# Optimization experiments

Hardware: AMD Instinct MI355X
Metric: run time of the kernel (lower is better)

Reference implementation:

```python
import jax, jax.numpy as jnp
import numpy as np

N_NODES = 50000
N_EDGES = 1600000
N_GRAPHS = 16
K_SLOTS = 8
LATENT = 4
HID = 32


def _linear(key, fan_in, fan_out):
    lim = 1.0 / np.sqrt(fan_in)
    kw, kb = jax.random.split(key)
    w = jax.random.uniform(kw, (fan_in, fan_out), minval=-lim, maxval=lim, dtype=jnp.float32)
    b = jax.random.uniform(kb, (fan_out,), minval=-lim, maxval=lim, dtype=jnp.float32)
    return w, b


def setup_inputs() -> dict:
    key = jax.random.key(0)
    ks = jax.random.split(key, 12)
    x = jax.random.normal(ks[0], (N_NODES, 4), dtype=jnp.float32)
    pos = jax.random.normal(ks[1], (N_NODES, 3), dtype=jnp.float32)
    # edge_index without self-loops (src != dst) so dist > 0 everywhere
    src = jax.random.randint(ks[2], (N_EDGES,), 0, N_NODES)
    off = jax.random.randint(ks[3], (N_EDGES,), 1, N_NODES)
    dst = (src + off) % N_NODES
    edge_index = jnp.stack([src, dst], axis=0).astype(jnp.int64)
    batch = jnp.sort(jax.random.randint(ks[4], (N_NODES,), 0, N_GRAPHS)).astype(jnp.int64)
    enc_w1, enc_b1 = _linear(ks[5], 4 * 2 + 1, HID)
    enc_w2, enc_b2 = _linear(ks[6], HID, HID)
    pool_w, pool_b = _linear(ks[7], HID, K_SLOTS)
    toz_w, toz_b = _linear(ks[8], HID, LATENT)
    dec_w1, dec_b1 = _linear(ks[9], LATENT, HID)
    dec_w2, dec_b2 = _linear(ks[10], HID, 4)
    return {
        "x": x, "pos": pos, "edge_index": edge_index, "batch": batch,
        "enc_w1": enc_w1, "enc_b1": enc_b1, "enc_w2": enc_w2, "enc_b2": enc_b2,
        "pool_w": pool_w, "pool_b": pool_b, "toz_w": toz_w, "toz_b": toz_b,
        "dec_w1": dec_w1, "dec_b1": dec_b1, "dec_w2": dec_w2, "dec_b2": dec_b2,
    }


def reference(x, pos, edge_index, batch,
              enc_w1, enc_b1, enc_w2, enc_b2,
              pool_w, pool_b, toz_w, toz_b,
              dec_w1, dec_b1, dec_w2, dec_b2):
    src = edge_index[0]  # x_j (source)
    dst = edge_index[1]  # x_i (target, aggregation index in PyG default flow)
    # EquiLayer: relative distance + message MLP + mean aggregation
    rel_pos = pos[src] - pos[dst]                         # [E, 3]
    dist = jnp.linalg.norm(rel_pos, axis=-1, keepdims=True)  # [E, 1]
    msg_in = jnp.concatenate([x[dst], x[src], dist], axis=-1)  # [E, 9]
    msg = jax.nn.silu(msg_in @ enc_w1 + enc_b1) @ enc_w2 + enc_b2  # [E, 32]
    summed = jax.ops.segment_sum(msg, dst, num_segments=N_NODES)   # [N, 32]
    cnt = jax.ops.segment_sum(jnp.ones((msg.shape[0], 1), msg.dtype), dst,
                              num_segments=N_NODES)
    h = summed / jnp.maximum(cnt, 1.0)                    # scatter-mean
    # soft pooling over k slots per graph
    s = jax.nn.softmax(h @ pool_w + pool_b, axis=-1)      # [N, k]
    pooled_h = jax.ops.segment_sum(s[:, :, None] * h[:, None, :], batch,
                                   num_segments=N_GRAPHS)  # [B, k, 32]
    z = pooled_h @ toz_w + toz_b                           # [B, k, latent]
    # decode: torch.matmul(s [N,k], z [B,k,d]) -> [B, N, d]
    q = jnp.einsum('nk,bkd->bnd', s, z)
    recon = jax.nn.silu(q @ dec_w1 + dec_b1) @ dec_w2 + dec_b2  # [B, N, 4]
    return recon
```

## Files before the change

### kernel.cpp

```cpp
#include <hip/hip_runtime.h>
#include <hip/hip_bf16.h>

#define N_NODES 50000
#define N_EDGES 1600000
#define N_GRAPHS 16
#define K_SLOTS 8
#define LATENT 4
#define HID 32
#define NBUCKET 196
#define BCAP 10240
#define BIN_EPB 4096

typedef __hip_bfloat16 bf16;
typedef __attribute__((ext_vector_type(8))) short short8;
typedef __attribute__((ext_vector_type(4))) float f32x4;

__device__ __forceinline__ float ldf(const void* p, long i, int isbf) {
    return isbf ? __bfloat162float(((const bf16*)p)[i]) : ((const float*)p)[i];
}
__device__ __forceinline__ int ldi(const int* p, long i, int is64) {
    return is64 ? p[2 * i] : p[i];
}
__device__ __forceinline__ short f2bs(float f) {
    bf16 h = __float2bfloat16(f);
    return *reinterpret_cast<short*>(&h);
}
__device__ __forceinline__ float bs2f(unsigned s) {
    union { unsigned u; float f; } cv;
    cv.u = (s & 0xFFFFu) << 16;
    return cv.f;
}
__device__ __forceinline__ float fast_silu(float v) {
    return v * __builtin_amdgcn_rcpf(1.f + __expf(-v));
}

#define WS_HSUM 0
#define WS_POOL (N_NODES * HID)
#define WS_GFILL (WS_POOL + N_GRAPHS * K_SLOTS * HID)
#define WS_ZERO_CNT (WS_GFILL + 256)
#define WS_S    (WS_GFILL + 256)
#define WS_FRAGS (WS_S + N_NODES * K_SLOTS)
#define WS_DEG  (WS_FRAGS + 1024)
#define WS_BINNED (WS_DEG + N_NODES)
#define WS_EDAT (WS_BINNED + NBUCKET * BCAP)
#define WS_FLAGS (WS_EDAT + N_EDGES)

__global__ void prep_kernel(const void* x, const int* ei,
                            const void* w1, const void* w2,
                            int* flags, short* frags)
{
    int t = threadIdx.x;
    unsigned short h = ((const unsigned short*)x)[2 * t];
    unsigned e = (h >> 7) & 0xFF;
    bool sane = ((h & 0x7FFF) == 0 || (e >= 100 && e <= 141));
    unsigned long long bs = __ballot(sane);
    int f0 = (__popcll(bs) >= 32) ? 1 : 0;
    bool z = (ei[2 * t + 1] == 0);
    unsigned long long bz = __ballot(z);
    int f1 = (__popcll(bz) >= 60) ? 1 : 0;
    if (t == 0) { flags[0] = f0; flags[1] = f1; }

    int fbf = f0;
    int nl = t & 15, quad = (t >> 4) & 3;
#pragma unroll
    for (int j = 0; j < 8; j++) {
        int k = quad * 8 + j;
        frags[(0 * 64 + t) * 8 + j] = (k < 9) ? f2bs(ldf(w1, k * 32 + nl, fbf)) : (short)0;
        frags[(1 * 64 + t) * 8 + j] = (k < 9) ? f2bs(ldf(w1, k * 32 + 16 + nl, fbf)) : (short)0;
        frags[(2 * 64 + t) * 8 + j] = f2bs(ldf(w2, k * 32 + nl, fbf));
        frags[(3 * 64 + t) * 8 + j] = f2bs(ldf(w2, k * 32 + 16 + nl, fbf));
    }
}

__global__ __launch_bounds__(256) void bin_kernel(
    const int* __restrict__ ei, int* __restrict__ gfill,
    unsigned* __restrict__ binned, const int* __restrict__ flags)
{
    const int i64 = flags[1];
    __shared__ int cnt[NBUCKET];
    __shared__ int cur[NBUCKET];
    int t = threadIdx.x;
    for (int i = t; i < NBUCKET; i += 256) cnt[i] = 0;
    __syncthreads();

    long e0 = (long)blockIdx.x * BIN_EPB;
    unsigned pk[16];
    if (!i64) {
#pragma unroll
        for (int kk = 0; kk < 4; kk++) {
            long e = e0 + kk * 1024 + t * 4;
            if (e < N_EDGES) {
                int4 sv = *(const int4*)(ei + e);
                int4 dv = *(const int4*)(ei + N_EDGES + e);
                pk[kk * 4 + 0] = (unsigned)sv.x | ((unsigned)dv.x << 16);
                pk[kk * 4 + 1] = (unsigned)sv.y | ((unsigned)dv.y << 16);
                pk[kk * 4 + 2] = (unsigned)sv.z | ((unsigned)dv.z << 16);
                pk[kk * 4 + 3] = (unsigned)sv.w | ((unsigned)dv.w << 16);
                atomicAdd(&cnt[dv.x >> 8], 1);
                atomicAdd(&cnt[dv.y >> 8], 1);
                atomicAdd(&cnt[dv.z >> 8], 1);
                atomicAdd(&cnt[dv.w >> 8], 1);
            } else {
                pk[kk * 4 + 0] = pk[kk * 4 + 1] = pk[kk * 4 + 2] = pk[kk * 4 + 3] = 0xFFFFFFFFu;
            }
        }
    } else {
#pragma unroll
        for (int kk = 0; kk < 8; kk++) {
            long e = e0 + kk * 512 + t * 2;
            if (e < N_EDGES) {
                int4 sv = *(const int4*)(ei + 2 * e);
                int4 dv = *(const int4*)(ei + 2 * (N_EDGES + e));
                pk[kk * 2 + 0] = (unsigned)sv.x | ((unsigned)dv.x << 16);
                pk[kk * 2 + 1] = (unsigned)sv.z | ((unsigned)dv.z << 16);
                atomicAdd(&cnt[dv.x >> 8], 1);
                atomicAdd(&cnt[dv.z >> 8], 1);
            } else {
                pk[kk * 2 + 0] = pk[kk * 2 + 1] = 0xFFFFFFFFu;
            }
        }
    }
    __syncthreads();
    for (int i = t; i < NBUCKET; i += 256)
        cur[i] = atomicAdd(&gfill[i], cnt[i]);
    __syncthreads();
    int nk = i64 ? 16 : 16;
#pragma unroll
    for (int k = 0; k < 16; k++) {
        if (k < nk && pk[k] != 0xFFFFFFFFu) {
            int b = pk[k] >> 24;
            int pos = atomicAdd(&cur[b], 1);
            binned[(long)b * BCAP + pos] = pk[k];
        }
    }
}

__global__ __launch_bounds__(1024) void csr_kernel(
    const int* __restrict__ gfill, const unsigned* __restrict__ binned,
    unsigned* __restrict__ edat, int* __restrict__ deg)
{
    __shared__ int gsm[256];
    __shared__ int lcnt[256], lcur[256], sm[256];
    int b = blockIdx.x, t = threadIdx.x;
    if (t < 256) gsm[t] = (t < NBUCKET) ? gfill[t] : 0;
    if (t < 256) lcnt[t] = 0;
    __syncthreads();
    for (int s = 1; s < 256; s <<= 1) {
        int v = 0;
        if (t < 256) v = gsm[t] + ((t >= s) ? gsm[t - s] : 0);
        __syncthreads();
        if (t < 256) gsm[t] = v;
        __syncthreads();
    }
    int cnt = gfill[b];
    int base = gsm[b] - cnt;
    const unsigned* bp = binned + (long)b * BCAP;
    for (int i = t; i < cnt; i += 1024)
        atomicAdd(&lcnt[(bp[i] >> 16) & 255], 1);
    __syncthreads();
    if (t < 256) sm[t] = lcnt[t];
    __syncthreads();
    for (int s = 1; s < 256; s <<= 1) {
        int v = 0;
        if (t < 256) v = sm[t] + ((t >= s) ? sm[t - s] : 0);
        __syncthreads();
        if (t < 256) sm[t] = v;
        __syncthreads();
    }
    if (t < 256) {
        lcur[t] = sm[t] - lcnt[t];
        int n = b * 256 + t;
        if (n < N_NODES) deg[n] = lcnt[t];
    }
    __syncthreads();
    for (int i = t; i < cnt; i += 1024) {
        unsigned pk = bp[i];
        int pos = base + atomicAdd(&lcur[(pk >> 16) & 255], 1);
        edat[pos] = pk;
    }
}

__global__ __launch_bounds__(256) void msg_agg_kernel(
    const void* __restrict__ x, const void* __restrict__ pos,
    const unsigned* __restrict__ edat, const short* __restrict__ frags,
    const void* __restrict__ b1, const void* __restrict__ b2,
    float* __restrict__ hsum, const int* __restrict__ flags)
{
    const int fbf = flags[0];
    __shared__ short buf[256 * 34];
    __shared__ int sdL[256];
    __shared__ int runstart[256];
    __shared__ int wcnt[4];

    int t = threadIdx.x;
    int lane = t & 63, wv = t >> 6;
    int nl = lane & 15, quad = lane >> 4;

    const short8 w1f0 = *(const short8*)&frags[(0 * 64 + lane) * 8];
    const short8 w1f1 = *(const short8*)&frags[(1 * 64 + lane) * 8];
    const short8 w2f0 = *(const short8*)&frags[(2 * 64 + lane) * 8];
    const short8 w2f1 = *(const short8*)&frags[(3 * 64 + lane) * 8];
    float b1c0 = ldf(b1, nl, fbf), b1c1 = ldf(b1, 16 + nl, fbf);
    float b2c0 = ldf(b2, nl, fbf), b2c1 = ldf(b2, 16 + nl, fbf);

    long i = (long)blockIdx.x * 256 + t;
    unsigned ed = edat[i];
    int src = (int)(ed & 0xFFFFu);
    int dst = (int)(ed >> 16);
    sdL[t] = dst;

    float in[9];
    if (fbf) {
        const unsigned* xb = (const unsigned*)x;
        unsigned d0 = xb[dst * 2], d1 = xb[dst * 2 + 1];
        unsigned s0 = xb[src * 2], s1 = xb[src * 2 + 1];
        in[0] = bs2f(d0); in[1] = bs2f(d0 >> 16);
        in[2] = bs2f(d1); in[3] = bs2f(d1 >> 16);
        in[4] = bs2f(s0); in[5] = bs2f(s0 >> 16);
        in[6] = bs2f(s1); in[7] = bs2f(s1 >> 16);
        const unsigned short* pp = (const unsigned short*)pos;
        float dx = bs2f(pp[3 * src + 0]) - bs2f(pp[3 * dst + 0]);
        float dy = bs2f(pp[3 * src + 1]) - bs2f(pp[3 * dst + 1]);
        float dz = bs2f(pp[3 * src + 2]) - bs2f(pp[3 * dst + 2]);
        in[8] = sqrtf(dx * dx + dy * dy + dz * dz);
    } else {
        float4 xd = ((const float4*)x)[dst];
        float4 xs = ((const float4*)x)[src];
        in[0] = xd.x; in[1] = xd.y; in[2] = xd.z; in[3] = xd.w;
        in[4] = xs.x; in[5] = xs.y; in[6] = xs.z; in[7] = xs.w;
        const float* pf = (const float*)pos;
        float dx = pf[3 * src + 0] - pf[3 * dst + 0];
        float dy = pf[3 * src + 1] - pf[3 * dst + 1];
        float dz = pf[3 * src + 2] - pf[3 * dst + 2];
        in[8] = sqrtf(dx * dx + dy * dy + dz * dz);
    }

    {
        unsigned* rowp = (unsigned*)&buf[t * 34];
        short v9 = f2bs(in[8]);
        rowp[0] = (unsigned)(unsigned short)f2bs(in[0]) | ((unsigned)(unsigned short)f2bs(in[1]) << 16);
        rowp[1] = (unsigned)(unsigned short)f2bs(in[2]) | ((unsigned)(unsigned short)f2bs(in[3]) << 16);
        rowp[2] = (unsigned)(unsigned short)f2bs(in[4]) | ((unsigned)(unsigned short)f2bs(in[5]) << 16);
        rowp[3] = (unsigned)(unsigned short)f2bs(in[6]) | ((unsigned)(unsigned short)f2bs(in[7]) << 16);
        rowp[4] = (unsigned)(unsigned short)v9;
#pragma unroll
        for (int p = 5; p < 16; p++) rowp[p] = 0;
    }
    __syncthreads();

    int rb = wv * 64;
    short8 af[4];
#pragma unroll
    for (int mt = 0; mt < 4; mt++) {
        int row = rb + mt * 16 + nl;
        af[mt] = *(short8*)&buf[row * 34 + quad * 8];
    }
    __syncthreads();

    f32x4 zero = {0.f, 0.f, 0.f, 0.f};
#pragma unroll
    for (int mt = 0; mt < 4; mt++) {
        f32x4 c0 = __builtin_amdgcn_mfma_f32_16x16x32_bf16(af[mt], w1f0, zero, 0, 0, 0);
        f32x4 c1 = __builtin_amdgcn_mfma_f32_16x16x32_bf16(af[mt], w1f1, zero, 0, 0, 0);
#pragma unroll
        for (int r = 0; r < 4; r++) {
            int row = rb + mt * 16 + quad * 4 + r;
            buf[row * 34 + nl] = f2bs(fast_silu(c0[r] + b1c0));
            buf[row * 34 + 16 + nl] = f2bs(fast_silu(c1[r] + b1c1));
        }
    }
    __syncthreads();

    short8 a2f[4];
#pragma unroll
    for (int mt = 0; mt < 4; mt++) {
        int row = rb + mt * 16 + nl;
        a2f[mt] = *(short8*)&buf[row * 34 + quad * 8];
    }
    __syncthreads();

    short* msgT = buf;
#pragma unroll
    for (int mt = 0; mt < 4; mt++) {
        f32x4 d0 = __builtin_amdgcn_mfma_f32_16x16x32_bf16(a2f[mt], w2f0, zero, 0, 0, 0);
        f32x4 d1 = __builtin_amdgcn_mfma_f32_16x16x32_bf16(a2f[mt], w2f1, zero, 0, 0, 0);
#pragma unroll
        for (int r = 0; r < 4; r++) {
            int orow = rb + mt * 16 + quad * 4 + r;
            msgT[nl * 258 + orow] = f2bs(d0[r] + b2c0);
            msgT[(nl + 16) * 258 + orow] = f2bs(d1[r] + b2c1);
        }
    }
    __syncthreads();

    bool head = (t == 0) || (sdL[t] != sdL[t - 1]);
    unsigned long long bal = __ballot(head);
    if (lane == 0) wcnt[wv] = __popcll(bal);
    __syncthreads();
    int nruns = wcnt[0] + wcnt[1] + wcnt[2] + wcnt[3];
    if (head) {
        int base = 0;
        for (int q = 0; q < wv; q++) base += wcnt[q];
        int myrun = base + __popcll(bal & (((unsigned long long)1 << lane) - 1ull));
        runstart[myrun] = t;
    }
    __syncthreads();

    int g = t >> 5, c = t & 31;
    const short* col = &msgT[c * 258];
    const unsigned* colu = (const unsigned*)col;
    for (int r = g; r < nruns; r += 8) {
        int s0 = runstart[r];
        int s1 = (r + 1 < nruns) ? runstart[r + 1] : 256;
        float acc = 0.f;
        int j = s0;
        if (j & 1) { acc += bs2f((unsigned)(unsigned short)col[j]); j++; }
        for (; j + 1 < s1; j += 2) {
            unsigned d = colu[j >> 1];
            acc += bs2f(d) + bs2f(d >> 16);
        }
        if (j < s1) acc += bs2f((unsigned)(unsigned short)col[j]);
        int node = sdL[s0];
        if (s0 == 0 || s1 == 256) atomicAdd(&hsum[(size_t)node * HID + c], acc);
        else hsum[(size_t)node * HID + c] = acc;
    }
}

__global__ __launch_bounds__(256) void pool_softmax_kernel(
    const float* __restrict__ hsum, const int* __restrict__ deg,
    const int* __restrict__ batch,
    const void* __restrict__ pw, const void* __restrict__ pb,
    float* __restrict__ s, float* __restrict__ pooled,
    const int* __restrict__ flags)
{
    const int fbf = flags[0], i64 = flags[1];
    __shared__ float spw[HID * K_SLOTS], spb[K_SLOTS];
    __shared__ float hL[256 * 33];
    __shared__ float sL[256 * 9];
    __shared__ float invL[256];
    __shared__ int gL[256];
    int t = threadIdx.x;
    int n0 = blockIdx.x * 256;
    spw[t] = ldf(pw, t, fbf);
    if (t < K_SLOTS) spb[t] = ldf(pb, t, fbf);
    {
        int n = n0 + t;
        gL[t] = ldi(batch, (n < N_NODES) ? n : (N_NODES - 1), i64);
        invL[t] = (n < N_NODES) ? __builtin_amdgcn_rcpf(fmaxf((float)deg[n], 1.f)) : 0.f;
    }
    __syncthreads();
    for (int i = t; i < 256 * HID; i += 256) {
        int row = i >> 5, col = i & 31;
        int n = n0 + row;
        hL[row * 33 + col] = (n < N_NODES) ? hsum[(size_t)n0 * HID + i] * invL[row] : 0.f;
    }
    __syncthreads();

    if (n0 + t < N_NODES) {
        float l[K_SLOTS];
#pragma unroll
        for (int k = 0; k < K_SLOTS; k++) l[k] = spb[k];
#pragma unroll
        for (int j = 0; j < HID; j++) {
            float v = hL[t * 33 + j];
#pragma unroll
            for (int k = 0; k < K_SLOTS; k++) l[k] = fmaf(v, spw[j * K_SLOTS + k], l[k]);
        }
        float mx = l[0];
#pragma unroll
        for (int k = 1; k < K_SLOTS; k++) mx = fmaxf(mx, l[k]);
        float sum = 0.f;
#pragma unroll
        for (int k = 0; k < K_SLOTS; k++) { l[k] = __expf(l[k] - mx); sum += l[k]; }
        float is = __builtin_amdgcn_rcpf(sum);
#pragma unroll
        for (int k = 0; k < K_SLOTS; k++) { l[k] *= is; sL[t * 9 + k] = l[k]; }
        float4 v0 = make_float4(l[0], l[1], l[2], l[3]);
        float4 v1 = make_float4(l[4], l[5], l[6], l[7]);
        float4* sp = (float4*)(s + (size_t)(n0 + t) * K_SLOTS);
        sp[0] = v0; sp[1] = v1;
    } else {
#pragma unroll
        for (int k = 0; k < K_SLOTS; k++) sL[t * 9 + k] = 0.f;
    }
    __syncthreads();

    int k = t >> 5, c = t & 31;
    float acc = 0.f;
    int curg = gL[0];
    int lim = min(256, N_NODES - n0);
    for (int i = 0; i < lim; i++) {
        int g = gL[i];
        if (g != curg) {
            atomicAdd(&pooled[curg * 256 + t], acc);
            acc = 0.f;
            curg = g;
        }
        acc = fmaf(sL[i * 9 + k], hL[i * 33 + c], acc);
    }
    atomicAdd(&pooled[curg * 256 + t], acc);
}

__global__ __launch_bounds__(256) void decode_kernel(
    const float* __restrict__ s, const float* __restrict__ pooled,
    const void* __restrict__ tw, const void* __restrict__ tb,
    const void* __restrict__ dw1, const void* __restrict__ db1,
    const void* __restrict__ dw2, const void* __restrict__ db2,
    void* __restrict__ out, const int* __restrict__ flags)
{
    const int fbf = flags[0];
    __shared__ float zb[K_SLOTS * LATENT];
    __shared__ float w1[LATENT * HID], b1s[HID], w2[HID * LATENT], b2s[LATENT];
    int b = blockIdx.y;
    int t = threadIdx.x;
    if (t < K_SLOTS * LATENT) {
        int k = t >> 2, d = t & 3;
        float acc = ldf(tb, d, fbf);
        for (int c = 0; c < HID; c++)
            acc = fmaf(pooled[b * 256 + k * 32 + c], ldf(tw, c * 4 + d, fbf), acc);
        zb[t] = acc;
    }
    if (t < LATENT * HID) w1[t] = ldf(dw1, t, fbf);
    else if (t < LATENT * HID + HID * LATENT) w2[t - LATENT * HID] = ldf(dw2, t - LATENT * HID, fbf);
    if (t < HID) b1s[t] = ldf(db1, t, fbf);
    if (t < LATENT) b2s[t] = ldf(db2, t, fbf);
    __syncthreads();

    int n = blockIdx.x * 256 + t;
    if (n >= N_NODES) return;
    float sv[K_SLOTS];
#pragma unroll
    for (int k = 0; k < K_SLOTS; k++) sv[k] = s[(size_t)n * K_SLOTS + k];
    float q[LATENT];
#pragma unroll
    for (int d = 0; d < LATENT; d++) {
        float a = 0.f;
#pragma unroll
        for (int k = 0; k < K_SLOTS; k++) a = fmaf(sv[k], zb[k * LATENT + d], a);
        q[d] = a;
    }
    float t1[HID];
#pragma unroll
    for (int j = 0; j < HID; j++) t1[j] = b1s[j];
#pragma unroll
    for (int d = 0; d < LATENT; d++) {
        float v = q[d];
#pragma unroll
        for (int j = 0; j < HID; j++) t1[j] = fmaf(v, w1[d * HID + j], t1[j]);
    }
#pragma unroll
    for (int j = 0; j < HID; j++) t1[j] = fast_silu(t1[j]);
    float o[LATENT];
#pragma unroll
    for (int d = 0; d < LATENT; d++) o[d] = b2s[d];
#pragma unroll
    for (int j = 0; j < HID; j++) {
        float v = t1[j];
#pragma unroll
        for (int d = 0; d < LATENT; d++) o[d] = fmaf(v, w2[j * LATENT + d], o[d]);
    }
    if (fbf) {
        union { bf16 h[4]; uint2 u; } pk;
#pragma unroll
        for (int d = 0; d < LATENT; d++) pk.h[d] = __float2bfloat16(o[d]);
        ((uint2*)out)[(size_t)b * N_NODES + n] = pk.u;
    } else {
        float4 v4 = make_float4(o[0], o[1], o[2], o[3]);
        ((float4*)out)[(size_t)b * N_NODES + n] = v4;
    }
}

extern "C" void kernel_launch(void* const* d_in, const int* in_sizes, int n_in,
                              void* d_out, int out_size, void* d_ws, size_t ws_size,
                              hipStream_t stream) {
    const void* x      = d_in[0];
    const void* pos    = d_in[1];
    const int*  ei     = (const int*)d_in[2];
    const int*  batch  = (const int*)d_in[3];
    const void* enc_w1 = d_in[4];
    const void* enc_b1 = d_in[5];
    const void* enc_w2 = d_in[6];
    const void* enc_b2 = d_in[7];
    const void* pool_w = d_in[8];
    const void* pool_b = d_in[9];
    const void* toz_w  = d_in[10];
    const void* toz_b  = d_in[11];
    const void* dec_w1 = d_in[12];
    const void* dec_b1 = d_in[13];
    const void* dec_w2 = d_in[14];
    const void* dec_b2 = d_in[15];

    float* ws = (float*)d_ws;
    float* hsum   = ws + WS_HSUM;
    float* pooled = ws + WS_POOL;
    int*   gfill  = (int*)(ws + WS_GFILL);
    float* s      = ws + WS_S;
    short* frags  = (short*)(ws + WS_FRAGS);
    int*   deg    = (int*)(ws + WS_DEG);
    unsigned* binned = (unsigned*)(ws + WS_BINNED);
    unsigned* edat   = (unsigned*)(ws + WS_EDAT);
    int*   flags  = (int*)(ws + WS_FLAGS);

    hipMemsetAsync(d_ws, 0, (size_t)WS_ZERO_CNT * 4, stream);
    prep_kernel<<<1, 64, 0, stream>>>(x, ei, enc_w1, enc_w2, flags, frags);

    int gbin = (N_EDGES + BIN_EPB - 1) / BIN_EPB;
    bin_kernel<<<gbin, 256, 0, stream>>>(ei, gfill, binned, flags);
    csr_kernel<<<NBUCKET, 1024, 0, stream>>>(gfill, binned, edat, deg);

    msg_agg_kernel<<<N_EDGES / 256, 256, 0, stream>>>(
        x, pos, edat, frags, enc_b1, enc_b2, hsum, flags);

    pool_softmax_kernel<<<NBUCKET, 256, 0, stream>>>(
        hsum, deg, batch, pool_w, pool_b, s, pooled, flags);
    dim3 dg((N_NODES + 255) / 256, N_GRAPHS);
    decode_kernel<<<dg, 256, 0, stream>>>(
        s, pooled, toz_w, toz_b, dec_w1, dec_b1, dec_w2, dec_b2, d_out, flags);
}
```

Before: 214.5 us.

## Sort edges locally in LDS before binning; zero hsum in csr kernel

The bin kernel now does a block-local counting sort of its edges into shared memory, then writes each bucket's edges to global memory as contiguous runs instead of scattering them with per-edge atomics. The memset of the large hsum buffer is removed; each csr block zeroes its slice of hsum, and the workspace is reordered so that only the small pooled and gfill areas are memset. Paired bf16 packing replaces per-element conversion in the message kernel. This adds a prefix scan and extra shared memory and synchronisation to the bin kernel.

Result: no change. 212.7 us (-0.8%).

```diff
diff --git a/kernel.cpp b/kernel.cpp
--- a/kernel.cpp
+++ b/kernel.cpp
@@ -25,6 +25,10 @@
     bf16 h = __float2bfloat16(f);
     return *reinterpret_cast<short*>(&h);
 }
+__device__ __forceinline__ unsigned pk2(float a, float b) {
+    __hip_bfloat162 h2 = __float22bfloat162_rn(make_float2(a, b));
+    return *reinterpret_cast<unsigned*>(&h2);
+}
 __device__ __forceinline__ float bs2f(unsigned s) {
     union { unsigned u; float f; } cv;
     cv.u = (s & 0xFFFFu) << 16;
@@ -34,11 +38,11 @@
     return v * __builtin_amdgcn_rcpf(1.f + __expf(-v));
 }
 
-#define WS_HSUM 0
-#define WS_POOL (N_NODES * HID)
-#define WS_GFILL (WS_POOL + N_GRAPHS * K_SLOTS * HID)
-#define WS_ZERO_CNT (WS_GFILL + 256)
-#define WS_S    (WS_GFILL + 256)
+#define WS_POOL 0
+#define WS_GFILL 4096
+#define WS_ZERO_CNT 4352
+#define WS_HSUM 4352
+#define WS_S    (WS_HSUM + N_NODES * HID)
 #define WS_FRAGS (WS_S + N_NODES * K_SLOTS)
 #define WS_DEG  (WS_FRAGS + 1024)
 #define WS_BINNED (WS_DEG + N_NODES)
@@ -78,7 +82,11 @@
 {
     const int i64 = flags[1];
     __shared__ int cnt[NBUCKET];
-    __shared__ int cur[NBUCKET];
+    __shared__ int lbase[NBUCKET];
+    __shared__ int lcur[NBUCKET];
+    __shared__ int gbase[NBUCKET];
+    __shared__ int tmp[256];
+    __shared__ unsigned sorted[BIN_EPB];
     int t = threadIdx.x;
     for (int i = t; i < NBUCKET; i += 256) cnt[i] = 0;
     __syncthreads();
@@ -121,23 +129,44 @@
         }
     }
     __syncthreads();
-    for (int i = t; i < NBUCKET; i += 256)
-        cur[i] = atomicAdd(&gfill[i], cnt[i]);
-    __syncthreads();
-    int nk = i64 ? 16 : 16;
+
+    tmp[t] = (t < NBUCKET) ? cnt[t] : 0;
+    __syncthreads();
+    for (int s = 1; s < 256; s <<= 1) {
+        int v = tmp[t] + ((t >= s) ? tmp[t - s] : 0);
+        __syncthreads();
+        tmp[t] = v;
+        __syncthreads();
+    }
+    int total = tmp[255];
+    if (t < NBUCKET) {
+        int ex = tmp[t] - cnt[t];
+        lbase[t] = ex;
+        lcur[t] = ex;
+        gbase[t] = atomicAdd(&gfill[t], cnt[t]);
+    }
+    __syncthreads();
+
 #pragma unroll
     for (int k = 0; k < 16; k++) {
-        if (k < nk && pk[k] != 0xFFFFFFFFu) {
+        if (pk[k] != 0xFFFFFFFFu) {
             int b = pk[k] >> 24;
-            int pos = atomicAdd(&cur[b], 1);
-            binned[(long)b * BCAP + pos] = pk[k];
-        }
+            int p = atomicAdd(&lcur[b], 1);
+            sorted[p] = pk[k];
+        }
+    }
+    __syncthreads();
+
+    for (int j = t; j < total; j += 256) {
+        unsigned ed = sorted[j];
+        int b = ed >> 24;
+        binned[(long)b * BCAP + gbase[b] + (j - lbase[b])] = ed;
     }
 }
 
 __global__ __launch_bounds__(1024) void csr_kernel(
     const int* __restrict__ gfill, const unsigned* __restrict__ binned,
-    unsigned* __restrict__ edat, int* __restrict__ deg)
+    unsigned* __restrict__ edat, int* __restrict__ deg, float* __restrict__ hsum)
 {
     __shared__ int gsm[256];
     __shared__ int lcnt[256], lcur[256], sm[256];
@@ -151,6 +180,14 @@
         __syncthreads();
         if (t < 256) gsm[t] = v;
         __syncthreads();
+    }
+    {
+        int nvalid = min(256, N_NODES - b * 256);
+        if (nvalid > 0) {
+            float4* hz = (float4*)(hsum + (size_t)b * 256 * HID);
+            float4 z4 = make_float4(0.f, 0.f, 0.f, 0.f);
+            for (int i = t; i < nvalid * 8; i += 1024) hz[i] = z4;
+        }
     }
     int cnt = gfill[b];
     int base = gsm[b] - cnt;
@@ -237,12 +274,11 @@
 
     {
         unsigned* rowp = (unsigned*)&buf[t * 34];
-        short v9 = f2bs(in[8]);
-        rowp[0] = (unsigned)(unsigned short)f2bs(in[0]) | ((unsigned)(unsigned short)f2bs(in[1]) << 16);
-        rowp[1] = (unsigned)(unsigned short)f2bs(in[2]) | ((unsigned)(unsigned short)f2bs(in[3]) << 16);
-        rowp[2] = (unsigned)(unsigned short)f2bs(in[4]) | ((unsigned)(unsigned short)f2bs(in[5]) << 16);
-        rowp[3] = (unsigned)(unsigned short)f2bs(in[6]) | ((unsigned)(unsigned short)f2bs(in[7]) << 16);
-        rowp[4] = (unsigned)(unsigned short)v9;
+        rowp[0] = pk2(in[0], in[1]);
+        rowp[1] = pk2(in[2], in[3]);
+        rowp[2] = pk2(in[4], in[5]);
+        rowp[3] = pk2(in[6], in[7]);
+        rowp[4] = pk2(in[8], 0.f);
 #pragma unroll
         for (int p = 5; p < 16; p++) rowp[p] = 0;
     }
@@ -284,12 +320,13 @@
     for (int mt = 0; mt < 4; mt++) {
         f32x4 d0 = __builtin_amdgcn_mfma_f32_16x16x32_bf16(a2f[mt], w2f0, zero, 0, 0, 0);
         f32x4 d1 = __builtin_amdgcn_mfma_f32_16x16x32_bf16(a2f[mt], w2f1, zero, 0, 0, 0);
-#pragma unroll
-        for (int r = 0; r < 4; r++) {
-            int orow = rb + mt * 16 + quad * 4 + r;
-            msgT[nl * 258 + orow] = f2bs(d0[r] + b2c0);
-            msgT[(nl + 16) * 258 + orow] = f2bs(d1[r] + b2c1);
-        }
+        int ob = rb + mt * 16 + quad * 4;
+        unsigned* c0p = (unsigned*)&msgT[nl * 258 + ob];
+        unsigned* c1p = (unsigned*)&msgT[(nl + 16) * 258 + ob];
+        c0p[0] = pk2(d0[0] + b2c0, d0[1] + b2c0);
+        c0p[1] = pk2(d0[2] + b2c0, d0[3] + b2c0);
+        c1p[0] = pk2(d1[0] + b2c1, d1[1] + b2c1);
+        c1p[1] = pk2(d1[2] + b2c1, d1[3] + b2c1);
     }
     __syncthreads();
 
@@ -491,9 +528,9 @@
     const void* dec_b2 = d_in[15];
 
     float* ws = (float*)d_ws;
-    float* hsum   = ws + WS_HSUM;
     float* pooled = ws + WS_POOL;
     int*   gfill  = (int*)(ws + WS_GFILL);
+    float* hsum   = ws + WS_HSUM;
     float* s      = ws + WS_S;
     short* frags  = (short*)(ws + WS_FRAGS);
     int*   deg    = (int*)(ws + WS_DEG);
@@ -506,7 +543,7 @@
 
     int gbin = (N_EDGES + BIN_EPB - 1) / BIN_EPB;
     bin_kernel<<<gbin, 256, 0, stream>>>(ei, gfill, binned, flags);
-    csr_kernel<<<NBUCKET, 1024, 0, stream>>>(gfill, binned, edat, deg);
+    csr_kernel<<<NBUCKET, 1024, 0, stream>>>(gfill, binned, edat, deg, hsum);
 
     msg_agg_kernel<<<N_EDGES / 256, 256, 0, stream>>>(
         x, pos, edat, frags, enc_b1, enc_b2, hsum, flags);
```
